# Kernel tuning notes

Hardware: AMD Instinct MI355X
Metric: run time of the kernel (lower is better)

Reference implementation:

```python
import jax, jax.numpy as jnp
import numpy as np
from jax.scipy.special import erf

# Module hyperparameters (from init_kwargs)
IN_C, OUT_C = 256, 512
IN_S, OUT_S = 196, 49
C_DIM, S_DIM = 512, 196        # lcm(256,512), lcm(196,49)
IN_CF, OUT_CF = 2, 1           # channel factors
IN_SF, OUT_SF = 1, 4           # spatio factors
NUM_POINTS = 5
NUM_STEPS = 3
STEP = 0.33333
BATCH = 256

# manet.func.sigmoid surrogates (all map R -> (0,1))
def ngd(x):   # normal gaussian distribution CDF
    return 0.5 * (1.0 + erf(x * 0.7071067811865476))

def nerf(x):  # normalized erf
    return 0.5 * (1.0 + erf(x))

def alg1(x):  # algebraic sigmoid, order 1
    return 0.5 * (x / (1.0 + jnp.abs(x))) + 0.5


def setup_inputs() -> dict:
    key = jax.random.key(0)
    ks = jax.random.split(key, 5)
    data = jax.random.normal(ks[0], (BATCH, IN_C, IN_S), dtype=jnp.float32)
    in_weight = jax.random.normal(ks[1], (1, C_DIM, S_DIM), dtype=jnp.float32)
    in_bias = jax.random.normal(ks[2], (1, C_DIM, S_DIM), dtype=jnp.float32)
    out_weight = jax.random.normal(ks[3], (1, C_DIM, S_DIM), dtype=jnp.float32)
    out_bias = jax.random.normal(ks[4], (1, C_DIM, S_DIM), dtype=jnp.float32)
    angles = jnp.linspace(0.0, 2.0 * np.pi, NUM_POINTS).astype(jnp.float32)
    velocity = jnp.linspace(0.0, 1.0, NUM_POINTS).astype(jnp.float32)
    return {"data": data, "in_weight": in_weight, "in_bias": in_bias,
            "out_weight": out_weight, "out_bias": out_bias,
            "angles": angles, "velocity": velocity}


def _clamped_bgn(index):
    # faithful reproduction of accessor() clamping arithmetic
    bgn = jnp.floor(index).astype(jnp.int32)
    bgn = bgn * (bgn >= 0)
    bgn = bgn * (bgn <= NUM_POINTS - 2) + (bgn - 1) * (bgn > NUM_POINTS - 2)
    bgn = bgn * (bgn <= NUM_POINTS - 2) + (bgn - 1) * (bgn > NUM_POINTS - 2)
    return bgn


def _access(memory, x, sig_fn):
    # data-dependent piecewise-linear LUT lookup
    index = sig_fn(x) * NUM_POINTS
    bgn = _clamped_bgn(index)
    pos = index - bgn
    return (1.0 - pos) * memory[bgn] + pos * memory[bgn + 1]


def reference(data, in_weight, in_bias, out_weight, out_bias, angles, velocity):
    # expansion: [B, Cin, Sin] -> [B, C_DIM, S_DIM]
    x = data.reshape(-1, IN_C, 1, IN_S, 1)
    x = x * in_weight.reshape(1, IN_C, IN_CF, IN_S, IN_SF)
    x = x + in_bias.reshape(1, IN_C, IN_CF, IN_S, IN_SF)
    x = x.reshape(-1, C_DIM, S_DIM)

    # nonlinear: iterative MAC step; note step() itself multiplies by STEP,
    # and nonlinear() multiplies the step output by STEP again -> STEP*STEP.
    for _ in range(NUM_STEPS):
        ang = _access(angles, x, ngd)
        vel = _access(velocity, x, nerf)
        x = x + (vel * jnp.cos(ang) + x * vel * jnp.sin(ang)) * (STEP * STEP)

    # attention gate
    att = alg1(x * out_weight + out_bias)
    x = x * att

    # reduction: [B, C_DIM, S_DIM] -> [B, OUT_C, OUT_S]
    x = x.reshape(-1, OUT_CF, OUT_C, OUT_SF, OUT_S)
    return jnp.sum(x, axis=(1, 3))
```

## Files before the change

### kernel.cpp

```cpp
#include <hip/hip_runtime.h>
#include <hip/hip_fp16.h>


#define STEP2f    0.11110889f
#define INV_2PI   0.15915494309189535f
#define LOG2E     1.4426950408889634f
#define LUT_N     4096
#define LUT_B     8.0f
#define LUT_SCALE 256.0f
#define BPT       8

struct MacCoef {
    float ca1, ca3, cb1, cb3;
    float A0r, dAr;
    float V0s, dVs;
};

__device__ __forceinline__ MacCoef make_coef(const float* angles, const float* velocity) {
    MacCoef c;
    c.ca1 = -1.5957691216f * LOG2E;
    c.ca3 = -0.0713548168f * LOG2E;
    c.cb1 = c.ca1 * 1.41421356237f;
    c.cb3 = c.ca3 * 2.82842712475f;
    c.A0r = angles[0] * INV_2PI;
    c.dAr = (angles[4] - angles[0]) * 1.25f * INV_2PI;
    c.V0s = velocity[0] * STEP2f;
    c.dVs = (velocity[4] - velocity[0]) * 1.25f * STEP2f;
    return c;
}

__device__ __forceinline__ float mac_step(float x, const MacCoef& c) {
    float xx = x * x;
    float ua = fminf(x * fmaf(c.ca3, xx, c.ca1), 60.0f);
    float ub = fminf(x * fmaf(c.cb3, xx, c.cb1), 60.0f);
    float ea = __builtin_amdgcn_exp2f(ua);
    float eb = __builtin_amdgcn_exp2f(ub);
    float da = 1.0f + ea, db = 1.0f + eb;
    float rp = __builtin_amdgcn_rcpf(da * db);
    float sa = db * rp;
    float sb = da * rp;
    float r  = fmaf(c.dAr, sa, c.A0r);
    float v2 = fmaf(c.dVs, sb, c.V0s);
    float sn = __builtin_amdgcn_sinf(r);
    float cs = __builtin_amdgcn_cosf(r);
    return fmaf(v2, fmaf(x, sn, cs), x);
}

__device__ __forceinline__ float F3(float x, const MacCoef& c) {
    x = mac_step(x, c);
    x = mac_step(x, c);
    return mac_step(x, c);
}

__global__ __launch_bounds__(256) void build_lut(
    const float* __restrict__ angles, const float* __restrict__ velocity,
    __half2* __restrict__ lut2)
{
    int i = blockIdx.x * 256 + threadIdx.x;
    if (i >= LUT_N) return;
    MacCoef c = make_coef(angles, velocity);
    float x0 = fmaf((float)i,       1.0f / LUT_SCALE, -LUT_B);
    float x1 = fmaf((float)(i + 1), 1.0f / LUT_SCALE, -LUT_B);
    lut2[i] = __halves2half2(__float2half(F3(x0, c)), __float2half(F3(x1, c)));
}

__global__ __launch_bounds__(256) void mac_kernel(
    const float* __restrict__ data,
    const float* __restrict__ in_w,
    const float* __restrict__ in_b,
    const float* __restrict__ out_w,
    const float* __restrict__ out_b,
    const float* __restrict__ angles,
    const float* __restrict__ velocity,
    const __half2* __restrict__ glut,
    float* __restrict__ out)
{
    __shared__ __half2 lut[LUT_N];

    const int tid = threadIdx.x;
    {
        const uint4* src = (const uint4*)glut;
        uint4* dst = (uint4*)lut;
#pragma unroll
        for (int i = 0; i < 4; ++i) dst[tid + 256 * i] = src[tid + 256 * i];
    }

    const int t  = blockIdx.x * 256 + tid;
    const int os = t % 49;
    const int cc = t / 49;
    const int wbase = cc * 196;

    MacCoef c = make_coef(angles, velocity);
    float snp = __builtin_amdgcn_sinf(c.A0r + c.dAr);
    float cP  = fmaf(c.V0s + c.dVs, snp, 1.0f);
    float slopeP = cP * cP * cP;
    float snn = __builtin_amdgcn_sinf(c.A0r);
    float cN  = fmaf(c.V0s, snn, 1.0f);
    float slopeN = cN * cN * cN;

    float iw[4], ib[4], ow[4], ob[4];
#pragma unroll
    for (int sf = 0; sf < 4; ++sf) {
        int s = wbase + sf * 49 + os;
        iw[sf] = in_w[s];  ib[sf] = in_b[s];
        ow[sf] = out_w[s]; ob[sf] = out_b[s];
    }

    __syncthreads();

#pragma unroll
    for (int k = 0; k < BPT; ++k) {
        const int b = blockIdx.y * BPT + k;
        const int dbase = (b * 256 + (cc >> 1)) * 196;

        float y[4], tg[4];
#pragma unroll
        for (int sf = 0; sf < 4; ++sf) {
            float x0 = fmaf(data[dbase + sf * 49 + os], iw[sf], ib[sf]);
            float xc = fminf(fmaxf(x0, -LUT_B), LUT_B);
            float fi = fmaf(xc, LUT_SCALE, 2048.0f);
            int   j  = min((int)fi, LUT_N - 1);
            float fr = fi - (float)j;
            __half2 p = lut[j];
            float lo = __low2float(p), hi = __high2float(p);
            float v  = fmaf(fr, hi - lo, lo);
            float dd = x0 - xc;
            float sl = x0 > 0.0f ? slopeP : slopeN;
            y[sf]  = fmaf(dd, sl, v);
            tg[sf] = fmaf(y[sf], ow[sf], ob[sf]);
        }

        float acc = 0.0f;
#pragma unroll
        for (int p = 0; p < 2; ++p) {
            float d0 = 1.0f + fabsf(tg[2 * p]);
            float d1 = 1.0f + fabsf(tg[2 * p + 1]);
            float rr = __builtin_amdgcn_rcpf(d0 * d1);
            float a0 = fmaf(0.5f * tg[2 * p],     d1 * rr, 0.5f);
            float a1 = fmaf(0.5f * tg[2 * p + 1], d0 * rr, 0.5f);
            acc = fmaf(y[2 * p], a0, acc);
            acc = fmaf(y[2 * p + 1], a1, acc);
        }

        out[b * 25088 + t] = acc;
    }
}

extern "C" void kernel_launch(void* const* d_in, const int* in_sizes, int n_in,
                              void* d_out, int out_size, void* d_ws, size_t ws_size,
                              hipStream_t stream) {
    const float* data   = (const float*)d_in[0];
    const float* in_w   = (const float*)d_in[1];
    const float* in_b   = (const float*)d_in[2];
    const float* out_w  = (const float*)d_in[3];
    const float* out_b  = (const float*)d_in[4];
    const float* angles = (const float*)d_in[5];
    const float* vel    = (const float*)d_in[6];
    float* out = (float*)d_out;
    __half2* lut = (__half2*)d_ws;

    build_lut<<<dim3(LUT_N / 256), 256, 0, stream>>>(angles, vel, lut);

    dim3 grid(98, 256 / BPT);
    mac_kernel<<<grid, 256, 0, stream>>>(data, in_w, in_b, out_w, out_b,
                                         angles, vel, lut, out);
}
```

Measured before the change: 115.9 us.

## Process both channel-expansion outputs per thread and prefetch next batch row

Each thread now handles one input channel and produces both expanded output channels (cf=0,1), so each data element is loaded once instead of twice. The grid is halved in x, and each block writes two output channels per input channel. The next batch element's inputs are software-prefetched into registers, and outputs use nontemporal stores. This roughly doubles per-thread weight registers and halves the number of blocks, which reduces parallelism on a GPU with many CUs.

```diff
diff --git a/kernel.cpp b/kernel.cpp
--- a/kernel.cpp
+++ b/kernel.cpp
@@ -87,62 +87,83 @@
 
     const int t  = blockIdx.x * 256 + tid;
     const int os = t % 49;
-    const int cc = t / 49;
-    const int wbase = cc * 196;
+    const int c  = t / 49;
 
-    MacCoef c = make_coef(angles, velocity);
-    float snp = __builtin_amdgcn_sinf(c.A0r + c.dAr);
-    float cP  = fmaf(c.V0s + c.dVs, snp, 1.0f);
+    MacCoef mc = make_coef(angles, velocity);
+    float snp = __builtin_amdgcn_sinf(mc.A0r + mc.dAr);
+    float cP  = fmaf(mc.V0s + mc.dVs, snp, 1.0f);
     float slopeP = cP * cP * cP;
-    float snn = __builtin_amdgcn_sinf(c.A0r);
-    float cN  = fmaf(c.V0s, snn, 1.0f);
+    float snn = __builtin_amdgcn_sinf(mc.A0r);
+    float cN  = fmaf(mc.V0s, snn, 1.0f);
     float slopeN = cN * cN * cN;
 
-    float iw[4], ib[4], ow[4], ob[4];
+    float iw[2][4], ib[2][4], ow[2][4], ob[2][4];
+    const int wb = c * 392 + os;
 #pragma unroll
-    for (int sf = 0; sf < 4; ++sf) {
-        int s = wbase + sf * 49 + os;
-        iw[sf] = in_w[s];  ib[sf] = in_b[s];
-        ow[sf] = out_w[s]; ob[sf] = out_b[s];
-    }
+    for (int e = 0; e < 2; ++e)
+#pragma unroll
+        for (int sf = 0; sf < 4; ++sf) {
+            int s = wb + e * 196 + sf * 49;
+            iw[e][sf] = in_w[s];  ib[e][sf] = in_b[s];
+            ow[e][sf] = out_w[s]; ob[e][sf] = out_b[s];
+        }
 
     __syncthreads();
 
+    const float* dptr = data + ((size_t)(blockIdx.y * BPT) * 256 + c) * 196 + os;
+    float*       optr = out  + (size_t)(blockIdx.y * BPT) * 25088 + c * 98 + os;
+
+    float cur[4], nxt[4];
+#pragma unroll
+    for (int sf = 0; sf < 4; ++sf) cur[sf] = dptr[sf * 49];
+
 #pragma unroll
     for (int k = 0; k < BPT; ++k) {
-        const int b = blockIdx.y * BPT + k;
-        const int dbase = (b * 256 + (cc >> 1)) * 196;
+        if (k + 1 < BPT) {
+            const float* dn = dptr + (k + 1) * 50176;
+#pragma unroll
+            for (int sf = 0; sf < 4; ++sf) nxt[sf] = dn[sf * 49];
+        }
 
-        float y[4], tg[4];
+        float yv[2][4], tg[2][4];
 #pragma unroll
         for (int sf = 0; sf < 4; ++sf) {
-            float x0 = fmaf(data[dbase + sf * 49 + os], iw[sf], ib[sf]);
-            float xc = fminf(fmaxf(x0, -LUT_B), LUT_B);
-            float fi = fmaf(xc, LUT_SCALE, 2048.0f);
-            int   j  = min((int)fi, LUT_N - 1);
-            float fr = fi - (float)j;
-            __half2 p = lut[j];
-            float lo = __low2float(p), hi = __high2float(p);
-            float v  = fmaf(fr, hi - lo, lo);
-            float dd = x0 - xc;
-            float sl = x0 > 0.0f ? slopeP : slopeN;
-            y[sf]  = fmaf(dd, sl, v);
-            tg[sf] = fmaf(y[sf], ow[sf], ob[sf]);
+            float xv = cur[sf];
+#pragma unroll
+            for (int e = 0; e < 2; ++e) {
+                float x0 = fmaf(xv, iw[e][sf], ib[e][sf]);
+                float xc = fminf(fmaxf(x0, -LUT_B), LUT_B);
+                float fi = fmaf(xc, LUT_SCALE, 2048.0f);
+                int   j  = min((int)fi, LUT_N - 1);
+                float fr = fi - (float)j;
+                __half2 p = lut[j];
+                float lo = __low2float(p), hi = __high2float(p);
+                float v  = fmaf(fr, hi - lo, lo);
+                float dd = x0 - xc;
+                float sl = x0 > 0.0f ? slopeP : slopeN;
+                float y  = fmaf(dd, sl, v);
+                yv[e][sf] = y;
+                tg[e][sf] = fmaf(y, ow[e][sf], ob[e][sf]);
+            }
         }
 
-        float acc = 0.0f;
 #pragma unroll
-        for (int p = 0; p < 2; ++p) {
-            float d0 = 1.0f + fabsf(tg[2 * p]);
-            float d1 = 1.0f + fabsf(tg[2 * p + 1]);
-            float rr = __builtin_amdgcn_rcpf(d0 * d1);
-            float a0 = fmaf(0.5f * tg[2 * p],     d1 * rr, 0.5f);
-            float a1 = fmaf(0.5f * tg[2 * p + 1], d0 * rr, 0.5f);
-            acc = fmaf(y[2 * p], a0, acc);
-            acc = fmaf(y[2 * p + 1], a1, acc);
+        for (int e = 0; e < 2; ++e) {
+            float acc = 0.0f;
+#pragma unroll
+            for (int p = 0; p < 2; ++p) {
+                float t0 = tg[e][2 * p], t1 = tg[e][2 * p + 1];
+                float d0 = 1.0f + fabsf(t0);
+                float d1 = 1.0f + fabsf(t1);
+                float rr = __builtin_amdgcn_rcpf(d0 * d1);
+                acc = fmaf(yv[e][2 * p],     fmaf(0.5f * t0, d1 * rr, 0.5f), acc);
+                acc = fmaf(yv[e][2 * p + 1], fmaf(0.5f * t1, d0 * rr, 0.5f), acc);
+            }
+            __builtin_nontemporal_store(acc, optr + (size_t)k * 25088 + e * 49);
         }
 
-        out[b * 25088 + t] = acc;
+#pragma unroll
+        for (int sf = 0; sf < 4; ++sf) cur[sf] = nxt[sf];
     }
 }
 
@@ -161,7 +182,7 @@
 
     build_lut<<<dim3(LUT_N / 256), 256, 0, stream>>>(angles, vel, lut);
 
-    dim3 grid(98, 256 / BPT);
+    dim3 grid(49, 256 / BPT);
     mac_kernel<<<grid, 256, 0, stream>>>(data, in_w, in_b, out_w, out_b,
                                          angles, vel, lut, out);
 }
```

Measured after the change: 113.5 us. -2.1%, faster.
